# Kernel optimization log

Hardware: AMD Instinct MI355X
Metric: run time of the kernel (lower is better)

Reference implementation:

```python
import jax, jax.numpy as jnp
import numpy as np

B = 8192
D = 1024
NUM_CLASSES = 128
EPS = 1e-8  # torch F.cosine_similarity default eps


def setup_inputs() -> dict:
    key = jax.random.key(0)
    k1, k2, k3 = jax.random.split(key, 3)
    label_tensor = jax.random.randint(k1, (B,), 0, NUM_CLASSES, dtype=jnp.int64 if jax.config.jax_enable_x64 else jnp.int32)
    feature_a = jax.random.normal(k2, (B, D), dtype=jnp.float32)
    feature_b = jax.random.normal(k3, (B, D), dtype=jnp.float32)
    return {"label_tensor": label_tensor, "feature_a": feature_a, "feature_b": feature_b}


def reference(label_tensor, feature_a, feature_b):
    # Pairwise cosine similarity: cos_score[i, k] = cos(a_i, b_k), shape [B, B]
    dots = feature_a @ feature_b.T  # [B, B]
    na = jnp.linalg.norm(feature_a, axis=1)  # [B]
    nb = jnp.linalg.norm(feature_b, axis=1)  # [B]
    cos_score = dots / jnp.maximum(na[:, None] * nb[None, :], EPS)
    # Row-softmax (torch softmax dim=1 on the [B, B] matrix)
    logp = jax.nn.log_softmax(cos_score, axis=1)
    # Label-equality mask: positives for row i are all j with same label
    mask = (label_tensor[:, None] == label_tensor[None, :]).astype(cos_score.dtype)  # [B, B]
    per_row = -(mask * logp).sum(axis=1) / mask.sum(axis=1)  # diagonal guarantees >=1 positive
    loss = per_row.mean()
    return loss, cos_score
```

## Files before the change

### kernel.cpp

```cpp
#include <hip/hip_runtime.h>
#include <hip/hip_bf16.h>

#define NB 8192
#define ND 1024

typedef __bf16 bf16x8 __attribute__((ext_vector_type(8)));
typedef float  f32x4  __attribute__((ext_vector_type(4)));

__device__ inline void gload_lds16(const void* g, void* l) {
    __builtin_amdgcn_global_load_lds(
        (const __attribute__((address_space(1))) unsigned int*)g,
        (__attribute__((address_space(3))) unsigned int*)l,
        16, 0, 0);
}

__device__ inline unsigned short f2bf(float x) {
    unsigned int u = __float_as_uint(x);
    return (unsigned short)((u + 0x7fffu + ((u >> 16) & 1u)) >> 16);
}

#define BARRIER() asm volatile("s_barrier" ::: "memory")
#define VMCNT(n)  asm volatile("s_waitcnt vmcnt(" #n ")" ::: "memory")
#define LGKM0()   do { asm volatile("s_waitcnt lgkmcnt(0)" ::: "memory"); \
                       __builtin_amdgcn_sched_barrier(0); } while (0)

__global__ __launch_bounds__(256) void prep_kernel(
    const float* __restrict__ A, const float* __restrict__ Bm,
    unsigned short* __restrict__ wa, unsigned short* __restrict__ wb,
    float* __restrict__ na, float* __restrict__ nb)
{
    int b = blockIdx.x;
    int wid = threadIdx.x >> 6, lane = threadIdx.x & 63;
    const float* src; unsigned short* dst; float* nrm; int row;
    if (b < 2048) { src = A;  dst = wa; nrm = na; row = b * 4 + wid; }
    else          { src = Bm; dst = wb; nrm = nb; row = (b - 2048) * 4 + wid; }

    const float*    rp = src + (size_t)row * ND;
    unsigned short* wp = dst + (size_t)row * ND;

    float ss = 0.f;
#pragma unroll
    for (int t = 0; t < 4; ++t) {
        int c = lane * 4 + t * 256;
        float4 v = *reinterpret_cast<const float4*>(rp + c);
        ss += v.x * v.x + v.y * v.y + v.z * v.z + v.w * v.w;
        ushort4 u;
        u.x = f2bf(v.x); u.y = f2bf(v.y); u.z = f2bf(v.z); u.w = f2bf(v.w);
        *reinterpret_cast<ushort4*>(wp + c) = u;
    }
#pragma unroll
    for (int off = 32; off; off >>= 1) ss += __shfl_xor(ss, off);
    if (lane == 0) nrm[row] = sqrtf(ss);
}

__global__ __launch_bounds__(256) void hist_kernel(
    const int* __restrict__ labels, int* __restrict__ hist)
{
    __shared__ int h[128];
    int tid = threadIdx.x;
    if (tid < 128) h[tid] = 0;
    __syncthreads();
    for (int i = tid; i < NB; i += 256) atomicAdd(&h[labels[i]], 1);
    __syncthreads();
    if (tid < 128) hist[tid] = h[tid];
}

__global__ __launch_bounds__(512, 2) void gemm_cos(
    const unsigned short* __restrict__ wa, const unsigned short* __restrict__ wb,
    const float* __restrict__ na, const float* __restrict__ nb,
    const int* __restrict__ labels,
    float* __restrict__ C, float* __restrict__ pe, float* __restrict__ pm)
{
    __shared__ unsigned short lds[4 * 16384];

    const int bid = blockIdx.x;
    const int tm  = (bid & 7) * 4 + ((bid >> 3) & 3);
    const int tn  = bid >> 5;

    const int tid  = threadIdx.x;
    const int lane = tid & 63;
    const int wid  = tid >> 6;
    const int wr   = wid >> 2, wc = wid & 3;
    const int l15  = lane & 15, lg = lane >> 4;

    const int m0 = tm * 256, n0 = tn * 256;

    const int srow = tid >> 2;
    const int sg   = (tid & 3) ^ ((tid >> 3) & 3);
    const unsigned short* gA = wa + (size_t)(m0 + srow) * ND + sg * 8;
    const unsigned short* gB = wb + (size_t)(n0 + srow) * ND + sg * 8;
    const int stA = wid * 512;

    const int kg  = ((lg ^ ((lane >> 1) & 3)) * 8);
    const int rdA = wr * 4096 + l15 * 32 + kg;
    const int rdB = 8192 + (wc >> 1) * 4096 + ((wc & 1) * 64 + l15) * 32 + kg;

    f32x4 acc[8][4];
#pragma unroll
    for (int i = 0; i < 8; ++i)
#pragma unroll
        for (int j = 0; j < 4; ++j) acc[i][j] = (f32x4){0.f, 0.f, 0.f, 0.f};

#define STAGE(t, X, h) gload_lds16( \
        (X ? gB : gA) + (size_t)(h) * 128 * ND + (t) * 32, \
        &lds[(((t) & 3) * 16384) + (X) * 8192 + (h) * 4096 + stA])

#define PHASE(t, q, SA, SB, ...) { \
    const int bufo = ((t) & 3) * 16384; \
    bf16x8 af[4], bq[4]; \
    _Pragma("unroll") \
    for (int m_ = 0; m_ < 4; ++m_) \
        af[m_] = *reinterpret_cast<const bf16x8*>(&lds[bufo + rdA + (q) * 2048 + m_ * 512]); \
    _Pragma("unroll") \
    for (int n_ = 0; n_ < 4; ++n_) \
        bq[n_] = *reinterpret_cast<const bf16x8*>(&lds[bufo + rdB + n_ * 512]); \
    if (SA) { STAGE((t) + 2, 0, 0); STAGE((t) + 2, 0, 1); } \
    if (SB) { STAGE((t) + 2, 1, 0); STAGE((t) + 2, 1, 1); } \
    BARRIER(); \
    LGKM0(); \
    __builtin_amdgcn_s_setprio(1); \
    _Pragma("unroll") \
    for (int m_ = 0; m_ < 4; ++m_) \
        _Pragma("unroll") \
        for (int n_ = 0; n_ < 4; ++n_) \
            acc[(q) * 4 + m_][n_] = __builtin_amdgcn_mfma_f32_16x16x32_bf16( \
                af[m_], bq[n_], acc[(q) * 4 + m_][n_], 0, 0, 0); \
    __builtin_amdgcn_s_setprio(0); \
    __VA_ARGS__; \
    BARRIER(); }

    STAGE(0, 0, 0); STAGE(0, 0, 1); STAGE(0, 1, 0); STAGE(0, 1, 1);
    STAGE(1, 0, 0); STAGE(1, 0, 1); STAGE(1, 1, 0); STAGE(1, 1, 1);
    VMCNT(4);
    BARRIER();

    for (int t = 0; t < 30; ++t) {
        PHASE(t, 0, 1, 0, (void)0);
        PHASE(t, 1, 0, 1, VMCNT(4));
    }
    PHASE(30, 0, 0, 0, (void)0);
    PHASE(30, 1, 0, 0, VMCNT(0));
    PHASE(31, 0, 0, 0, (void)0);
    PHASE(31, 1, 0, 0, (void)0);

#undef PHASE
#undef STAGE

    __syncthreads();
    float* pl = reinterpret_cast<float*>(lds);

    float nbv[4]; int labc[4];
#pragma unroll
    for (int n = 0; n < 4; ++n) {
        int c = n0 + wc * 64 + n * 16 + l15;
        nbv[n] = nb[c]; labc[n] = labels[c];
    }

#pragma unroll
    for (int m = 0; m < 8; ++m) {
#pragma unroll
        for (int jj = 0; jj < 4; ++jj) {
            int rl = wr * 128 + m * 16 + lg * 4 + jj;
            int r  = m0 + rl;
            float nav = na[r]; int labr = labels[r];
            float es = 0.f, ms = 0.f;
#pragma unroll
            for (int n = 0; n < 4; ++n) {
                int c = n0 + wc * 64 + n * 16 + l15;
                float v = acc[m][n][jj] / fmaxf(nav * nbv[n], 1e-8f);
                C[(size_t)r * NB + c] = v;
                es += __expf(v);
                ms += (labc[n] == labr) ? v : 0.f;
            }
#pragma unroll
            for (int off = 1; off < 16; off <<= 1) {
                es += __shfl_xor(es, off);
                ms += __shfl_xor(ms, off);
            }
            if (l15 == 0) {
                int o = (rl * 4 + wc) * 2;
                pl[o] = es; pl[o + 1] = ms;
            }
        }
    }
    __syncthreads();
    if (tid < 256) {
        float es = 0.f, ms = 0.f;
#pragma unroll
        for (int w = 0; w < 4; ++w) {
            es += pl[(tid * 4 + w) * 2];
            ms += pl[(tid * 4 + w) * 2 + 1];
        }
        int grow = m0 + tid;
        pe[tn * NB + grow] = es;
        pm[tn * NB + grow] = ms;
    }
}

__global__ __launch_bounds__(256) void loss_final(
    const float* __restrict__ pe, const float* __restrict__ pm,
    const int* __restrict__ labels, const int* __restrict__ hist,
    float* __restrict__ per_row)
{
    int row = blockIdx.x * 256 + threadIdx.x;
    float es = 0.f, ms = 0.f;
#pragma unroll
    for (int t = 0; t < 32; ++t) {
        es += pe[t * NB + row];
        ms += pm[t * NB + row];
    }
    per_row[row] = logf(es) - ms / (float)hist[labels[row]];
}

__global__ __launch_bounds__(256) void finalize(
    const float* __restrict__ per_row, float* __restrict__ out)
{
    __shared__ float sm[256];
    float s = 0.f;
    for (int i = threadIdx.x; i < NB; i += 256) s += per_row[i];
    sm[threadIdx.x] = s;
    __syncthreads();
    for (int k = 128; k; k >>= 1) {
        if (threadIdx.x < k) sm[threadIdx.x] += sm[threadIdx.x + k];
        __syncthreads();
    }
    if (threadIdx.x == 0) out[0] = sm[0] * (1.0f / (float)NB);
}

extern "C" void kernel_launch(void* const* d_in, const int* in_sizes, int n_in,
                              void* d_out, int out_size, void* d_ws, size_t ws_size,
                              hipStream_t stream) {
    const int*   labels = (const int*)d_in[0];
    const float* A      = (const float*)d_in[1];
    const float* Bm     = (const float*)d_in[2];
    float* out = (float*)d_out;

    char* ws = (char*)d_ws;
    unsigned short* wa = (unsigned short*)(ws);
    unsigned short* wb = (unsigned short*)(ws + 16777216);
    float* na      = (float*)(ws + 33554432);
    float* nb      = (float*)(ws + 33554432 + 32768);
    float* per_row = (float*)(ws + 33554432 + 65536);
    int*   hist    = (int*)  (ws + 33554432 + 98304);
    float* pe      = (float*)(ws + 33554432 + 131072);
    float* pm      = (float*)(ws + 33554432 + 131072 + 1048576);

    float* cosm = out + 1;

    prep_kernel<<<4096, 256, 0, stream>>>(A, Bm, wa, wb, na, nb);
    hist_kernel<<<1,    256, 0, stream>>>(labels, hist);
    gemm_cos   <<<1024, 512, 0, stream>>>(wa, wb, na, nb, labels, cosm, pe, pm);
    loss_final <<<32,   256, 0, stream>>>(pe, pm, labels, hist, per_row);
    finalize   <<<1,    256, 0, stream>>>(per_row, out);
}
```

Baseline: 261.5 us.

## Software-pipeline LDS fragment reads with double-buffered registers in GEMM main loop

Restructures the GEMM K-loop so the LDS fragment reads for the next half-step go into a second register set while MFMAs run on the current one. This removes the explicit lgkmcnt(0) wait and halves the per-K-step barriers. It also precomputes the second-half global pointers. In exchange it uses more VGPRs, since four fragment arrays are now live, which may pressure occupancy at 2 blocks per CU. It also relies on the compiler inserting correct waits for the LDS reads and on fewer barriers being enough to avoid buffer overwrite hazards.

```diff
diff --git a/kernel.cpp b/kernel.cpp
--- a/kernel.cpp
+++ b/kernel.cpp
@@ -21,8 +21,6 @@
 
 #define BARRIER() asm volatile("s_barrier" ::: "memory")
 #define VMCNT(n)  asm volatile("s_waitcnt vmcnt(" #n ")" ::: "memory")
-#define LGKM0()   do { asm volatile("s_waitcnt lgkmcnt(0)" ::: "memory"); \
-                       __builtin_amdgcn_sched_barrier(0); } while (0)
 
 __global__ __launch_bounds__(256) void prep_kernel(
     const float* __restrict__ A, const float* __restrict__ Bm,
@@ -87,8 +85,10 @@
 
     const int srow = tid >> 2;
     const int sg   = (tid & 3) ^ ((tid >> 3) & 3);
-    const unsigned short* gA = wa + (size_t)(m0 + srow) * ND + sg * 8;
-    const unsigned short* gB = wb + (size_t)(n0 + srow) * ND + sg * 8;
+    const unsigned short* gA0 = wa + (size_t)(m0 + srow) * ND + sg * 8;
+    const unsigned short* gA1 = gA0 + 128 * ND;
+    const unsigned short* gB0 = wb + (size_t)(n0 + srow) * ND + sg * 8;
+    const unsigned short* gB1 = gB0 + 128 * ND;
     const int stA = wid * 512;
 
     const int kg  = ((lg ^ ((lane >> 1) & 3)) * 8);
@@ -101,49 +101,72 @@
 #pragma unroll
         for (int j = 0; j < 4; ++j) acc[i][j] = (f32x4){0.f, 0.f, 0.f, 0.f};
 
+    bf16x8 af_a[4], af_b[4], bq_a[4], bq_b[4];
+
 #define STAGE(t, X, h) gload_lds16( \
-        (X ? gB : gA) + (size_t)(h) * 128 * ND + (t) * 32, \
+        (X ? (h ? gB1 : gB0) : (h ? gA1 : gA0)) + (t) * 32, \
         &lds[(((t) & 3) * 16384) + (X) * 8192 + (h) * 4096 + stA])
 
-#define PHASE(t, q, SA, SB, ...) { \
-    const int bufo = ((t) & 3) * 16384; \
-    bf16x8 af[4], bq[4]; \
-    _Pragma("unroll") \
+#define RD_A(dst, t, q) { _Pragma("unroll") \
     for (int m_ = 0; m_ < 4; ++m_) \
-        af[m_] = *reinterpret_cast<const bf16x8*>(&lds[bufo + rdA + (q) * 2048 + m_ * 512]); \
-    _Pragma("unroll") \
+        dst[m_] = *reinterpret_cast<const bf16x8*>( \
+            &lds[((t) & 3) * 16384 + rdA + (q) * 2048 + m_ * 512]); }
+
+#define RD_B(dst, t) { _Pragma("unroll") \
     for (int n_ = 0; n_ < 4; ++n_) \
-        bq[n_] = *reinterpret_cast<const bf16x8*>(&lds[bufo + rdB + n_ * 512]); \
-    if (SA) { STAGE((t) + 2, 0, 0); STAGE((t) + 2, 0, 1); } \
-    if (SB) { STAGE((t) + 2, 1, 0); STAGE((t) + 2, 1, 1); } \
-    BARRIER(); \
-    LGKM0(); \
+        dst[n_] = *reinterpret_cast<const bf16x8*>( \
+            &lds[((t) & 3) * 16384 + rdB + n_ * 512]); }
+
+#define MM(afx, bqx, q) { \
     __builtin_amdgcn_s_setprio(1); \
     _Pragma("unroll") \
     for (int m_ = 0; m_ < 4; ++m_) \
         _Pragma("unroll") \
         for (int n_ = 0; n_ < 4; ++n_) \
             acc[(q) * 4 + m_][n_] = __builtin_amdgcn_mfma_f32_16x16x32_bf16( \
-                af[m_], bq[n_], acc[(q) * 4 + m_][n_], 0, 0, 0); \
-    __builtin_amdgcn_s_setprio(0); \
-    __VA_ARGS__; \
-    BARRIER(); }
+                afx[m_], bqx[n_], acc[(q) * 4 + m_][n_], 0, 0, 0); \
+    __builtin_amdgcn_s_setprio(0); }
 
     STAGE(0, 0, 0); STAGE(0, 0, 1); STAGE(0, 1, 0); STAGE(0, 1, 1);
     STAGE(1, 0, 0); STAGE(1, 0, 1); STAGE(1, 1, 0); STAGE(1, 1, 1);
     VMCNT(4);
     BARRIER();
-
-    for (int t = 0; t < 30; ++t) {
-        PHASE(t, 0, 1, 0, (void)0);
-        PHASE(t, 1, 0, 1, VMCNT(4));
-    }
-    PHASE(30, 0, 0, 0, (void)0);
-    PHASE(30, 1, 0, 0, VMCNT(0));
-    PHASE(31, 0, 0, 0, (void)0);
-    PHASE(31, 1, 0, 0, (void)0);
-
-#undef PHASE
+    RD_B(bq_a, 0); RD_A(af_a, 0, 0);
+
+#pragma unroll
+    for (int tp = 0; tp < 15; ++tp) {
+        const int t = 2 * tp;
+        RD_A(af_b, t, 1);
+        STAGE(t + 2, 0, 0); STAGE(t + 2, 0, 1);
+        MM(af_a, bq_a, 0);
+        VMCNT(2);
+        BARRIER();
+        RD_B(bq_b, t + 1); RD_A(af_a, t + 1, 0);
+        STAGE(t + 2, 1, 0); STAGE(t + 2, 1, 1);
+        MM(af_b, bq_a, 1);
+        RD_A(af_b, t + 1, 1);
+        STAGE(t + 3, 0, 0); STAGE(t + 3, 0, 1);
+        MM(af_a, bq_b, 0);
+        VMCNT(2);
+        BARRIER();
+        RD_B(bq_a, t + 2); RD_A(af_a, t + 2, 0);
+        STAGE(t + 3, 1, 0); STAGE(t + 3, 1, 1);
+        MM(af_b, bq_b, 1);
+    }
+
+    RD_A(af_b, 30, 1);
+    MM(af_a, bq_a, 0);
+    VMCNT(0);
+    BARRIER();
+    RD_B(bq_b, 31); RD_A(af_a, 31, 0);
+    MM(af_b, bq_a, 1);
+    RD_A(af_b, 31, 1);
+    MM(af_a, bq_b, 0);
+    MM(af_b, bq_b, 1);
+
+#undef MM
+#undef RD_B
+#undef RD_A
 #undef STAGE
 
     __syncthreads();
```

After: 244.5 us. 1.07x faster.

## Restructure GEMM main loop to double-buffered BK=64 tiles with new swizzle

Applied to the files above, without the earlier changes.

The bf16 GEMM main loop moves from a 4-deep ring of K=32 LDS tiles to two K=64 buffers, each filled by 16-byte global_load_lds transfers into a row layout with an 8-way XOR swizzle. B fragments are loaded once per K-substep and reused across both M halves, which cuts LDS reads. Waits on outstanding loads drop to a single vmcnt(0) once per buffer rather than partial waits each K step. This reduces loop and barrier overhead per K, but the prefetch distance is shorter and the full drain may expose global load latency.

```diff
diff --git a/kernel.cpp b/kernel.cpp
--- a/kernel.cpp
+++ b/kernel.cpp
@@ -20,7 +20,7 @@
 }
 
 #define BARRIER() asm volatile("s_barrier" ::: "memory")
-#define VMCNT(n)  asm volatile("s_waitcnt vmcnt(" #n ")" ::: "memory")
+#define VMCNT0()  asm volatile("s_waitcnt vmcnt(0)" ::: "memory")
 #define LGKM0()   do { asm volatile("s_waitcnt lgkmcnt(0)" ::: "memory"); \
                        __builtin_amdgcn_sched_barrier(0); } while (0)
 
@@ -71,7 +71,7 @@
     const int* __restrict__ labels,
     float* __restrict__ C, float* __restrict__ pe, float* __restrict__ pm)
 {
-    __shared__ unsigned short lds[4 * 16384];
+    __shared__ unsigned short lds[65536];
 
     const int bid = blockIdx.x;
     const int tm  = (bid & 7) * 4 + ((bid >> 3) & 3);
@@ -85,15 +85,16 @@
 
     const int m0 = tm * 256, n0 = tn * 256;
 
-    const int srow = tid >> 2;
-    const int sg   = (tid & 3) ^ ((tid >> 3) & 3);
-    const unsigned short* gA = wa + (size_t)(m0 + srow) * ND + sg * 8;
-    const unsigned short* gB = wb + (size_t)(n0 + srow) * ND + sg * 8;
-    const int stA = wid * 512;
-
-    const int kg  = ((lg ^ ((lane >> 1) & 3)) * 8);
-    const int rdA = wr * 4096 + l15 * 32 + kg;
-    const int rdB = 8192 + (wc >> 1) * 4096 + ((wc & 1) * 64 + l15) * 32 + kg;
+    const int srow6 = tid >> 3;
+    const int sgr   = (tid & 7) ^ (srow6 & 7);
+    const unsigned short* pA = wa + (size_t)(m0 + srow6) * ND + sgr * 8;
+    const unsigned short* pB = wb + (size_t)(n0 + srow6) * ND + sgr * 8;
+    const int stW = wid * 512;
+    const int ND64 = 64 * ND;
+
+    const int swz0  = ((((l15 >> 2) & 1) << 2) | (lg ^ (l15 & 3))) * 8;
+    const int baseA = (wr * 128 + l15) * 64 + swz0;
+    const int baseB = 16384 + (wc * 64 + l15) * 64 + swz0;
 
     f32x4 acc[8][4];
 #pragma unroll
@@ -101,21 +102,25 @@
 #pragma unroll
         for (int j = 0; j < 4; ++j) acc[i][j] = (f32x4){0.f, 0.f, 0.f, 0.f};
 
-#define STAGE(t, X, h) gload_lds16( \
-        (X ? gB : gA) + (size_t)(h) * 128 * ND + (t) * 32, \
-        &lds[(((t) & 3) * 16384) + (X) * 8192 + (h) * 4096 + stA])
-
-#define PHASE(t, q, SA, SB, ...) { \
-    const int bufo = ((t) & 3) * 16384; \
-    bf16x8 af[4], bq[4]; \
+    bf16x8 bq[4];
+
+#define STG4(P, DST) do { \
+    gload_lds16((P),            &lds[(DST) + 0 * 4096 + stW]); \
+    gload_lds16((P) +     ND64, &lds[(DST) + 1 * 4096 + stW]); \
+    gload_lds16((P) + 2 * ND64, &lds[(DST) + 2 * 4096 + stW]); \
+    gload_lds16((P) + 3 * ND64, &lds[(DST) + 3 * 4096 + stW]); } while (0)
+
+#define PH(BUFB, KS, MH, RB, GATE, ...) { \
+    if (RB) { _Pragma("unroll") \
+        for (int n_ = 0; n_ < 4; ++n_) \
+            bq[n_] = *reinterpret_cast<const bf16x8*>( \
+                &lds[(BUFB) + ((baseB + n_ * 1024) ^ ((KS) * 32))]); } \
+    bf16x8 af[4]; \
     _Pragma("unroll") \
     for (int m_ = 0; m_ < 4; ++m_) \
-        af[m_] = *reinterpret_cast<const bf16x8*>(&lds[bufo + rdA + (q) * 2048 + m_ * 512]); \
-    _Pragma("unroll") \
-    for (int n_ = 0; n_ < 4; ++n_) \
-        bq[n_] = *reinterpret_cast<const bf16x8*>(&lds[bufo + rdB + n_ * 512]); \
-    if (SA) { STAGE((t) + 2, 0, 0); STAGE((t) + 2, 0, 1); } \
-    if (SB) { STAGE((t) + 2, 1, 0); STAGE((t) + 2, 1, 1); } \
+        af[m_] = *reinterpret_cast<const bf16x8*>( \
+            &lds[(BUFB) + ((baseA + ((MH) * 4 + m_) * 1024) ^ ((KS) * 32))]); \
+    __VA_ARGS__; \
     BARRIER(); \
     LGKM0(); \
     __builtin_amdgcn_s_setprio(1); \
@@ -123,28 +128,40 @@
     for (int m_ = 0; m_ < 4; ++m_) \
         _Pragma("unroll") \
         for (int n_ = 0; n_ < 4; ++n_) \
-            acc[(q) * 4 + m_][n_] = __builtin_amdgcn_mfma_f32_16x16x32_bf16( \
-                af[m_], bq[n_], acc[(q) * 4 + m_][n_], 0, 0, 0); \
+            acc[(MH) * 4 + m_][n_] = __builtin_amdgcn_mfma_f32_16x16x32_bf16( \
+                af[m_], bq[n_], acc[(MH) * 4 + m_][n_], 0, 0, 0); \
     __builtin_amdgcn_s_setprio(0); \
-    __VA_ARGS__; \
+    if (GATE) VMCNT0(); \
     BARRIER(); }
 
-    STAGE(0, 0, 0); STAGE(0, 0, 1); STAGE(0, 1, 0); STAGE(0, 1, 1);
-    STAGE(1, 0, 0); STAGE(1, 0, 1); STAGE(1, 1, 0); STAGE(1, 1, 1);
-    VMCNT(4);
+    STG4(pA, 0); STG4(pB, 16384);
+    VMCNT0();
     BARRIER();
 
-    for (int t = 0; t < 30; ++t) {
-        PHASE(t, 0, 1, 0, (void)0);
-        PHASE(t, 1, 0, 1, VMCNT(4));
-    }
-    PHASE(30, 0, 0, 0, (void)0);
-    PHASE(30, 1, 0, 0, VMCNT(0));
-    PHASE(31, 0, 0, 0, (void)0);
-    PHASE(31, 1, 0, 0, (void)0);
-
-#undef PHASE
-#undef STAGE
+    for (int j = 0; j < 8; ++j) {
+        const unsigned short* s1 = pA + (2 * j + 1) * 64;
+        const unsigned short* t1 = pB + (2 * j + 1) * 64;
+        PH(0, 0, 0, 1, 0, STG4(s1, 32768))
+        PH(0, 0, 1, 0, 0, STG4(t1, 32768 + 16384))
+        PH(0, 1, 0, 1, 0, (void)0)
+        PH(0, 1, 1, 0, 1, (void)0)
+        if (j < 7) {
+            const unsigned short* s2 = pA + (2 * j + 2) * 64;
+            const unsigned short* t2 = pB + (2 * j + 2) * 64;
+            PH(32768, 0, 0, 1, 0, STG4(s2, 0))
+            PH(32768, 0, 1, 0, 0, STG4(t2, 16384))
+            PH(32768, 1, 0, 1, 0, (void)0)
+            PH(32768, 1, 1, 0, 1, (void)0)
+        } else {
+            PH(32768, 0, 0, 1, 0, (void)0)
+            PH(32768, 0, 1, 0, 0, (void)0)
+            PH(32768, 1, 0, 1, 0, (void)0)
+            PH(32768, 1, 1, 0, 1, (void)0)
+        }
+    }
+
+#undef PH
+#undef STG4
 
     __syncthreads();
     float* pl = reinterpret_cast<float*>(lds);
```

Result: faster. 248.9 us (-4.8%).
